# Performance work log

Measured on AMD Instinct MI355X. Metric: run time of the kernel, lower is better.

Reference implementation:

```python
import jax, jax.numpy as jnp
import numpy as np

HEAD_COUNT = 16
EMBED_DIM = 2048
B, S = 2, 2048


def setup_inputs() -> dict:
    key = jax.random.key(0)
    k1, k2, k3, k4, k5 = jax.random.split(key, 5)
    keys = jax.random.normal(k1, (B, S, EMBED_DIM), dtype=jnp.float32)
    values = jax.random.normal(k2, (B, S, EMBED_DIM), dtype=jnp.float32)
    queries = jax.random.normal(k3, (B, S, EMBED_DIM), dtype=jnp.float32)
    # padding-style mask; guarantee at least one valid key per batch row
    attention_mask = jax.random.randint(k4, (B, S), 0, 2).astype(bool)
    attention_mask = attention_mask.at[:, 0].set(True)
    w_out = jax.random.normal(k5, (EMBED_DIM, EMBED_DIM), dtype=jnp.float32) * (EMBED_DIM ** -0.5)
    return {"keys": keys, "values": values, "queries": queries,
            "attention_mask": attention_mask, "w_out": w_out}


def reference(keys, values, queries, attention_mask, w_out):
    b, s, e = queries.shape
    h = HEAD_COUNT
    c = e // h  # head dim
    k = keys.reshape(b, s, h, c)
    v = values.reshape(b, s, h, c)
    q = queries.reshape(b, s, h, c) * (c ** -0.5)
    # [B,H,Q,K] scores + additive padding bias on key axis
    scores = jnp.einsum('bqhc,bkhc->bhqk', q, k)
    bias = jnp.where(attention_mask, 0.0, -jnp.inf)[:, None, None, :]
    weights = jax.nn.softmax(scores + bias, axis=-1)
    out = jnp.einsum('bhqk,bkhc->bqhc', weights, v).reshape(b, s, e)
    # nn.Linear(bias=False): y = x @ W^T
    return out @ w_out.T
```

## Files before the change

### kernel.cpp

```cpp
#include <hip/hip_runtime.h>
#include <hip/hip_bf16.h>
#include <math.h>

#define B_ 2
#define S_ 2048
#define E_ 2048
#define H_ 16
#define C_ 128

typedef __attribute__((ext_vector_type(8))) short s8v;
typedef __attribute__((ext_vector_type(4))) float f32x4;
typedef __attribute__((ext_vector_type(2))) unsigned u32x2;
typedef __attribute__((ext_vector_type(4))) unsigned u32x4;

#define MFMA16(a, b, c) __builtin_amdgcn_mfma_f32_16x16x32_bf16((a), (b), (c), 0, 0, 0)

__device__ __forceinline__ unsigned fbits(float f) {
    union { float f; unsigned u; } v{f};
    return v.u;
}
__device__ __forceinline__ short f2bfh(float f) {
    return (short)((fbits(f) + 0x8000u) >> 16);
}
__device__ __forceinline__ unsigned bfpack(float lo, float hi) {
    return __builtin_amdgcn_perm(fbits(hi) + 0x8000u, fbits(lo) + 0x8000u, 0x07060302u);
}

__device__ __forceinline__ void glds16(const void* g, void* l) {
    __builtin_amdgcn_global_load_lds(
        (const __attribute__((address_space(1))) void*)g,
        (__attribute__((address_space(3))) void*)l, 16, 0, 0);
}

template <bool DOK>
__global__ __launch_bounds__(256) void prep_kv(
    const float* __restrict__ K, const float* __restrict__ V,
    short* __restrict__ Kb, short* __restrict__ Vt)
{
    __shared__ __align__(16) short vt[C_][66];
    const int t  = threadIdx.x;
    const int s0 = blockIdx.x * 64;
    const int bh = blockIdx.y;
    const int b = bh >> 4, h = bh & 15;

    if (DOK) {
#pragma unroll
        for (int i = 0; i < 8; ++i) {
            int idx = t + i * 256;
            int s = idx >> 5, c4 = idx & 31;
            float4 v = *(const float4*)(K + ((size_t)(b * S_ + s0 + s)) * E_ + h * C_ + c4 * 4);
            u32x2 o = {bfpack(v.x, v.y), bfpack(v.z, v.w)};
            *(u32x2*)(Kb + ((size_t)(bh * S_ + s0 + s)) * C_ + c4 * 4) = o;
        }
    }
#pragma unroll
    for (int i = 0; i < 8; ++i) {
        int idx = t + i * 256;
        int r = idx >> 5, c4 = idx & 31;
        float4 v = *(const float4*)(V + ((size_t)(b * S_ + s0 + r)) * E_ + h * C_ + c4 * 4);
        vt[c4 * 4 + 0][r] = f2bfh(v.x);
        vt[c4 * 4 + 1][r] = f2bfh(v.y);
        vt[c4 * 4 + 2][r] = f2bfh(v.z);
        vt[c4 * 4 + 3][r] = f2bfh(v.w);
    }
    __syncthreads();
#pragma unroll
    for (int i = 0; i < 4; ++i) {
        int idx = t + i * 256;
        int c = idx >> 3, sc = idx & 7;
        *(s8v*)(Vt + ((size_t)(bh * C_ + c)) * S_ + s0 + sc * 8) = *(const s8v*)&vt[c][sc * 8];
    }
}

__global__ __launch_bounds__(256) void convw_kernel(
    const float* __restrict__ W, short* __restrict__ Wb)
{
    size_t i = ((size_t)blockIdx.x * 256 + threadIdx.x) * 8;
    float4 a = *(const float4*)(W + i);
    float4 b = *(const float4*)(W + i + 4);
    u32x4 o = {bfpack(a.x, a.y), bfpack(a.z, a.w), bfpack(b.x, b.y), bfpack(b.z, b.w)};
    *(u32x4*)(Wb + i) = o;
}

constexpr int QT = 128;
constexpr int KT = 64;
constexpr float M0 = 16.0f;

template <bool KBF16>
__global__ __launch_bounds__(256, 2) void attn_mfma(
    const short* __restrict__ Kb, const float* __restrict__ Kf,
    const float* __restrict__ Qp, const short* __restrict__ Vt,
    const int* __restrict__ maskp, short* __restrict__ Op)
{
    __shared__ __align__(16) short ks[2][KT * 128];
    __shared__ __align__(16) short vs[2][C_ * 64];
    __shared__ __align__(16) short ps[4][16][72];

    const int t = threadIdx.x;
    const int w = t >> 6, lane = t & 63;
    const int c15 = lane & 15, quad = lane >> 4;
    const int q0 = blockIdx.x * QT;
    const int h = blockIdx.y, b = blockIdx.z;
    const int bh = b * H_ + h;

    const float qscale = 0.12751744458187936f;
    s8v qf[2][4];
#pragma unroll
    for (int mi = 0; mi < 2; ++mi) {
        const float* qrow = Qp + ((size_t)(b * S_ + q0 + w * 32 + mi * 16 + c15)) * E_ + h * C_;
#pragma unroll
        for (int kk = 0; kk < 4; ++kk) {
            const float* p = qrow + kk * 32 + quad * 8;
            float4 x0 = *(const float4*)p;
            float4 x1 = *(const float4*)(p + 4);
            u32x4 pk = {bfpack(x0.x * qscale, x0.y * qscale),
                        bfpack(x0.z * qscale, x0.w * qscale),
                        bfpack(x1.x * qscale, x1.y * qscale),
                        bfpack(x1.z * qscale, x1.w * qscale)};
            qf[mi][kk] = *(s8v*)&pk;
        }
    }

    s8v ones;
#pragma unroll
    for (int j = 0; j < 8; ++j) ones[j] = (short)0x3F80;

    f32x4 O[2][8], Ol[2];
#pragma unroll
    for (int mi = 0; mi < 2; ++mi) {
        Ol[mi] = (f32x4){0.f, 0.f, 0.f, 0.f};
#pragma unroll
        for (int ct = 0; ct < 8; ++ct) O[mi][ct] = (f32x4){0.f, 0.f, 0.f, 0.f};
    }

    const short* Kbh = Kb + (size_t)(bh * S_) * C_;
    const float* Kfh = Kf + (size_t)(b * S_) * E_ + h * C_;
    const short* Vbh = Vt + (size_t)(bh * C_) * S_;
    const int*   mptr = maskp + b * S_ + 4 * c15;

    int kgp[4], vgp[2];
#pragma unroll
    for (int kk = 0; kk < 4; ++kk) kgp[kk] = ((4 * kk + quad) ^ c15) * 8;
#pragma unroll
    for (int ks2 = 0; ks2 < 2; ++ks2) vgp[ks2] = ((4 * ks2 + quad) ^ (c15 & 7)) * 8;

    auto stage = [&](short* ksb, short* vsb, int k0) {
        const int r4 = lane >> 4, gp = lane & 15;
#pragma unroll
        for (int i = 0; i < 4; ++i) {
            int row = w * 16 + i * 4 + r4;
            int g = gp ^ ((row >> 2) & 15);
            glds16(Kbh + (size_t)(k0 + row) * C_ + g * 8, ksb + (w * 16 + i * 4) * 128);
        }
        const int cr = lane >> 3, gp7 = lane & 7;
#pragma unroll
        for (int i = 0; i < 4; ++i) {
            int c = w * 32 + i * 8 + cr;
            int g = gp7 ^ (c & 7);
            glds16(Vbh + (size_t)c * S_ + k0 + g * 8, vsb + (w * 32 + i * 8) * 64);
        }
    };

    auto compute = [&](const short* ksc, const short* vsc, int4 mv) {
        float bva[4] = {mv.x ? -M0 : -1e30f, mv.y ? -M0 : -1e30f,
                        mv.z ? -M0 : -1e30f, mv.w ? -M0 : -1e30f};
        f32x4 Sf[2][4];
        __builtin_amdgcn_s_setprio(1);
#pragma unroll
        for (int nt = 0; nt < 4; ++nt) {
            f32x4 s0 = (f32x4){bva[nt], bva[nt], bva[nt], bva[nt]};
            f32x4 s1 = s0;
            const short* krow = ksc + (4 * c15 + nt) * 128;
#pragma unroll
            for (int kk = 0; kk < 4; ++kk) {
                s8v bf = *(const s8v*)(krow + kgp[kk]);
                s0 = MFMA16(qf[0][kk], bf, s0);
                s1 = MFMA16(qf[1][kk], bf, s1);
            }
            Sf[0][nt] = s0; Sf[1][nt] = s1;
        }
        __builtin_amdgcn_s_setprio(0);

        s8v af[2][2];
#pragma unroll
        for (int mi = 0; mi < 2; ++mi) {
#pragma unroll
            for (int r = 0; r < 4; ++r) {
                float p0 = exp2f(Sf[mi][0][r]);
                float p1 = exp2f(Sf[mi][1][r]);
                float p2 = exp2f(Sf[mi][2][r]);
                float p3 = exp2f(Sf[mi][3][r]);
                u32x2 d = {bfpack(p0, p1), bfpack(p2, p3)};
                *(u32x2*)&ps[w][quad * 4 + r][4 * c15] = d;
            }
#pragma unroll
            for (int ks2 = 0; ks2 < 2; ++ks2)
                af[mi][ks2] = *(const s8v*)&ps[w][c15][ks2 * 32 + quad * 8];
        }

        __builtin_amdgcn_s_setprio(1);
#pragma unroll
        for (int ct = 0; ct < 8; ++ct) {
            const short* vrow = vsc + (ct * 16 + c15) * 64;
#pragma unroll
            for (int ks2 = 0; ks2 < 2; ++ks2) {
                s8v bf = *(const s8v*)(vrow + vgp[ks2]);
                O[0][ct] = MFMA16(af[0][ks2], bf, O[0][ct]);
                O[1][ct] = MFMA16(af[1][ks2], bf, O[1][ct]);
            }
        }
#pragma unroll
        for (int mi = 0; mi < 2; ++mi) {
            Ol[mi] = MFMA16(af[mi][0], ones, Ol[mi]);
            Ol[mi] = MFMA16(af[mi][1], ones, Ol[mi]);
        }
        __builtin_amdgcn_s_setprio(0);
    };

    if (KBF16) {
        stage(&ks[0][0], &vs[0][0], 0);
        int4 mcur = *(const int4*)mptr;
        __syncthreads();
#pragma unroll 1
        for (int k0 = 0; k0 < S_; k0 += 2 * KT) {
            stage(&ks[1][0], &vs[1][0], k0 + KT);
            int4 m1 = *(const int4*)(mptr + k0 + KT);
            compute(&ks[0][0], &vs[0][0], mcur);
            __syncthreads();

            int4 m2 = m1;
            if (k0 + 2 * KT < S_) {
                stage(&ks[0][0], &vs[0][0], k0 + 2 * KT);
                m2 = *(const int4*)(mptr + k0 + 2 * KT);
            }
            compute(&ks[1][0], &vs[1][0], m1);
            mcur = m2;
            __syncthreads();
        }
    } else {
#pragma unroll 1
        for (int k0 = 0; k0 < S_; k0 += KT) {
#pragma unroll
            for (int i = 0; i < 8; ++i) {
                int idx = t + i * 256;
                int r = idx >> 5, c4 = idx & 31;
                float4 kv = *(const float4*)(Kfh + (size_t)(k0 + r) * E_ + c4 * 4);
                u32x2 sv = {bfpack(kv.x, kv.y), bfpack(kv.z, kv.w)};
                int gpw = (c4 >> 1) ^ ((r >> 2) & 15);
                *(u32x2*)&ks[0][r * 128 + gpw * 8 + (c4 & 1) * 4] = sv;
            }
            {
                const int cr = lane >> 3, gp7 = lane & 7;
#pragma unroll
                for (int i = 0; i < 4; ++i) {
                    int c = w * 32 + i * 8 + cr;
                    int g = gp7 ^ (c & 7);
                    glds16(Vbh + (size_t)c * S_ + k0 + g * 8, &vs[0][(w * 32 + i * 8) * 64]);
                }
            }
            int4 mv = *(const int4*)(mptr + k0);
            __syncthreads();
            compute(&ks[0][0], &vs[0][0], mv);
            __syncthreads();
        }
    }

#pragma unroll
    for (int mi = 0; mi < 2; ++mi) {
        float inv[4];
#pragma unroll
        for (int r = 0; r < 4; ++r) inv[r] = 1.f / Ol[mi][r];
        size_t rbase = (size_t)(b * S_ + q0 + w * 32 + mi * 16 + quad * 4) * E_ + h * C_;
#pragma unroll
        for (int ct = 0; ct < 8; ++ct)
#pragma unroll
            for (int r = 0; r < 4; ++r)
                Op[rbase + (size_t)r * E_ + ct * 16 + c15] = f2bfh(O[mi][ct][r] * inv[r]);
    }
}

template <bool WBF16>
__global__ __launch_bounds__(256, 2) void proj_mfma(
    const short* __restrict__ X, const short* __restrict__ Wb,
    const float* __restrict__ Wf, float* __restrict__ Y)
{
    __shared__ __align__(16) short As[2][128 * 64];
    __shared__ __align__(16) short Bs[2][128 * 64];

    const int t = threadIdx.x;
    const int w = t >> 6, lane = t & 63;
    const int c15 = lane & 15, quad = lane >> 4;
    const int bm = blockIdx.x * 128, bn = blockIdx.y * 128;
    const int wm = (w >> 1) * 64, wn = (w & 1) * 64;

    f32x4 acc[4][4];
#pragma unroll
    for (int mi = 0; mi < 4; ++mi)
#pragma unroll
        for (int ni = 0; ni < 4; ++ni) acc[mi][ni] = (f32x4){0.f, 0.f, 0.f, 0.f};

    int agp[2];
#pragma unroll
    for (int kk = 0; kk < 2; ++kk) agp[kk] = ((4 * kk + quad) ^ (c15 & 7)) * 8;

    auto stageAB = [&](short* Ab, short* Bb, int k0) {
        const int r8 = lane >> 3, gp = lane & 7;
#pragma unroll
        for (int i = 0; i < 4; ++i) {
            int row = w * 32 + i * 8 + r8;
            int g = gp ^ (row & 7);
            glds16(X + (size_t)(bm + row) * E_ + k0 + g * 8, Ab + (w * 32 + i * 8) * 64);
            glds16(Wb + (size_t)(bn + row) * E_ + k0 + g * 8, Bb + (w * 32 + i * 8) * 64);
        }
    };

    auto compute = [&](const short* Ab, const short* Bb) {
#pragma unroll
        for (int kk = 0; kk < 2; ++kk) {
            s8v a[4], bb[4];
#pragma unroll
            for (int mi = 0; mi < 4; ++mi)
                a[mi] = *(const s8v*)(Ab + (wm + mi * 16 + c15) * 64 + agp[kk]);
#pragma unroll
            for (int ni = 0; ni < 4; ++ni)
                bb[ni] = *(const s8v*)(Bb + (wn + ni * 16 + c15) * 64 + agp[kk]);
#pragma unroll
            for (int mi = 0; mi < 4; ++mi)
#pragma unroll
                for (int ni = 0; ni < 4; ++ni)
                    acc[mi][ni] = MFMA16(a[mi], bb[ni], acc[mi][ni]);
        }
    };

    if (WBF16) {
        stageAB(&As[0][0], &Bs[0][0], 0);
        __syncthreads();
#pragma unroll 1
        for (int k0 = 0; k0 < E_; k0 += 128) {
            stageAB(&As[1][0], &Bs[1][0], k0 + 64);
            compute(&As[0][0], &Bs[0][0]);
            __syncthreads();

            if (k0 + 128 < E_) stageAB(&As[0][0], &Bs[0][0], k0 + 128);
            compute(&As[1][0], &Bs[1][0]);
            __syncthreads();
        }
    } else {
#pragma unroll 1
        for (int k0 = 0; k0 < E_; k0 += 64) {
            {
                const int r8 = lane >> 3, gp = lane & 7;
#pragma unroll
                for (int i = 0; i < 4; ++i) {
                    int row = w * 32 + i * 8 + r8;
                    int g = gp ^ (row & 7);
                    glds16(X + (size_t)(bm + row) * E_ + k0 + g * 8, &As[0][(w * 32 + i * 8) * 64]);
                }
            }
#pragma unroll
            for (int i = 0; i < 8; ++i) {
                int idx = t + i * 256;
                int r = idx >> 4, c4 = idx & 15;
                float4 wv = *(const float4*)(Wf + (size_t)(bn + r) * E_ + k0 + c4 * 4);
                u32x2 sv = {bfpack(wv.x, wv.y), bfpack(wv.z, wv.w)};
                int gpw = (c4 >> 1) ^ (r & 7);
                *(u32x2*)&Bs[0][r * 64 + gpw * 8 + (c4 & 1) * 4] = sv;
            }
            __syncthreads();
            compute(&As[0][0], &Bs[0][0]);
            __syncthreads();
        }
    }

#pragma unroll
    for (int mi = 0; mi < 4; ++mi)
#pragma unroll
        for (int ni = 0; ni < 4; ++ni) {
            size_t rbase = (size_t)(bm + wm + mi * 16 + quad * 4) * E_ + bn + wn + ni * 16 + c15;
#pragma unroll
            for (int r = 0; r < 4; ++r) Y[rbase + (size_t)r * E_] = acc[mi][ni][r];
        }
}

extern "C" void kernel_launch(void* const* d_in, const int* in_sizes, int n_in,
                              void* d_out, int out_size, void* d_ws, size_t ws_size,
                              hipStream_t stream) {
    const float* keys    = (const float*)d_in[0];
    const float* values  = (const float*)d_in[1];
    const float* queries = (const float*)d_in[2];
    const int*   mask    = (const int*)d_in[3];
    const float* w_out   = (const float*)d_in[4];
    float* out = (float*)d_out;

    const size_t EL = (size_t)B_ * S_ * E_;
    short* ws  = (short*)d_ws;
    short* VtW = ws;
    short* Xb  = ws + EL;
    short* Kb  = ws + 2 * EL;
    short* Wb  = ws + 3 * EL;

    const bool hasK = ws_size >= (3 * EL) * 2;
    const bool hasW = ws_size >= (3 * EL + (size_t)E_ * E_) * 2;

    if (hasK)
        prep_kv<true><<<dim3(S_ / 64, B_ * H_), 256, 0, stream>>>(keys, values, Kb, VtW);
    else
        prep_kv<false><<<dim3(S_ / 64, B_ * H_), 256, 0, stream>>>(keys, values, Kb, VtW);
    if (hasW) convw_kernel<<<(E_ * E_ / 8) / 256, 256, 0, stream>>>(w_out, Wb);

    if (hasK)
        attn_mfma<true><<<dim3(S_ / QT, H_, B_), 256, 0, stream>>>(Kb, keys, queries, VtW, mask, Xb);
    else
        attn_mfma<false><<<dim3(S_ / QT, H_, B_), 256, 0, stream>>>(Kb, keys, queries, VtW, mask, Xb);

    if (hasW)
        proj_mfma<true><<<dim3((B_ * S_) / 128, E_ / 128), 256, 0, stream>>>(Xb, Wb, w_out, out);
    else
        proj_mfma<false><<<dim3((B_ * S_) / 128, E_ / 128), 256, 0, stream>>>(Xb, Wb, w_out, out);
}
```

Baseline: 281.6 us.

## Use 512-thread blocks with 16-row warps and drop K/V double buffering

The attention kernel moves from 4 waves handling 32 query rows each to 8 waves handling 16 rows each. It also replaces the double-buffered K/V LDS staging with a single buffer and two syncs per tile. The projection GEMM likewise uses 8 waves, each computing a 64x32 sub-tile. The aim is to cut registers per wave and raise occupancy, at the cost of less K-fragment reuse per wave, more syncs, and no overlap between loads and compute.

```diff
diff --git a/kernel.cpp b/kernel.cpp
--- a/kernel.cpp
+++ b/kernel.cpp
@@ -87,14 +87,14 @@
 constexpr float M0 = 16.0f;
 
 template <bool KBF16>
-__global__ __launch_bounds__(256, 2) void attn_mfma(
+__global__ __launch_bounds__(512, 4) void attn_mfma(
     const short* __restrict__ Kb, const float* __restrict__ Kf,
     const float* __restrict__ Qp, const short* __restrict__ Vt,
     const int* __restrict__ maskp, short* __restrict__ Op)
 {
-    __shared__ __align__(16) short ks[2][KT * 128];
-    __shared__ __align__(16) short vs[2][C_ * 64];
-    __shared__ __align__(16) short ps[4][16][72];
+    __shared__ __align__(16) short ks[KT * 128];
+    __shared__ __align__(16) short vs[C_ * 64];
+    __shared__ __align__(16) short ps[8][16][72];
 
     const int t = threadIdx.x;
     const int w = t >> 6, lane = t & 63;
@@ -104,10 +104,9 @@
     const int bh = b * H_ + h;
 
     const float qscale = 0.12751744458187936f;
-    s8v qf[2][4];
-#pragma unroll
-    for (int mi = 0; mi < 2; ++mi) {
-        const float* qrow = Qp + ((size_t)(b * S_ + q0 + w * 32 + mi * 16 + c15)) * E_ + h * C_;
+    s8v qf[4];
+    {
+        const float* qrow = Qp + ((size_t)(b * S_ + q0 + w * 16 + c15)) * E_ + h * C_;
 #pragma unroll
         for (int kk = 0; kk < 4; ++kk) {
             const float* p = qrow + kk * 32 + quad * 8;
@@ -117,7 +116,7 @@
                         bfpack(x0.z * qscale, x0.w * qscale),
                         bfpack(x1.x * qscale, x1.y * qscale),
                         bfpack(x1.z * qscale, x1.w * qscale)};
-            qf[mi][kk] = *(s8v*)&pk;
+            qf[kk] = *(s8v*)&pk;
         }
     }
 
@@ -125,13 +124,10 @@
 #pragma unroll
     for (int j = 0; j < 8; ++j) ones[j] = (short)0x3F80;
 
-    f32x4 O[2][8], Ol[2];
-#pragma unroll
-    for (int mi = 0; mi < 2; ++mi) {
-        Ol[mi] = (f32x4){0.f, 0.f, 0.f, 0.f};
-#pragma unroll
-        for (int ct = 0; ct < 8; ++ct) O[mi][ct] = (f32x4){0.f, 0.f, 0.f, 0.f};
-    }
+    f32x4 O[8], Ol;
+    Ol = (f32x4){0.f, 0.f, 0.f, 0.f};
+#pragma unroll
+    for (int ct = 0; ct < 8; ++ct) O[ct] = (f32x4){0.f, 0.f, 0.f, 0.f};
 
     const short* Kbh = Kb + (size_t)(bh * S_) * C_;
     const float* Kfh = Kf + (size_t)(b * S_) * E_ + h * C_;
@@ -144,143 +140,101 @@
 #pragma unroll
     for (int ks2 = 0; ks2 < 2; ++ks2) vgp[ks2] = ((4 * ks2 + quad) ^ (c15 & 7)) * 8;
 
-    auto stage = [&](short* ksb, short* vsb, int k0) {
-        const int r4 = lane >> 4, gp = lane & 15;
-#pragma unroll
-        for (int i = 0; i < 4; ++i) {
-            int row = w * 16 + i * 4 + r4;
-            int g = gp ^ ((row >> 2) & 15);
-            glds16(Kbh + (size_t)(k0 + row) * C_ + g * 8, ksb + (w * 16 + i * 4) * 128);
-        }
-        const int cr = lane >> 3, gp7 = lane & 7;
-#pragma unroll
-        for (int i = 0; i < 4; ++i) {
-            int c = w * 32 + i * 8 + cr;
-            int g = gp7 ^ (c & 7);
-            glds16(Vbh + (size_t)c * S_ + k0 + g * 8, vsb + (w * 32 + i * 8) * 64);
-        }
-    };
-
-    auto compute = [&](const short* ksc, const short* vsc, int4 mv) {
-        float bva[4] = {mv.x ? -M0 : -1e30f, mv.y ? -M0 : -1e30f,
-                        mv.z ? -M0 : -1e30f, mv.w ? -M0 : -1e30f};
-        f32x4 Sf[2][4];
-        __builtin_amdgcn_s_setprio(1);
-#pragma unroll
-        for (int nt = 0; nt < 4; ++nt) {
-            f32x4 s0 = (f32x4){bva[nt], bva[nt], bva[nt], bva[nt]};
-            f32x4 s1 = s0;
-            const short* krow = ksc + (4 * c15 + nt) * 128;
-#pragma unroll
-            for (int kk = 0; kk < 4; ++kk) {
-                s8v bf = *(const s8v*)(krow + kgp[kk]);
-                s0 = MFMA16(qf[0][kk], bf, s0);
-                s1 = MFMA16(qf[1][kk], bf, s1);
-            }
-            Sf[0][nt] = s0; Sf[1][nt] = s1;
-        }
-        __builtin_amdgcn_s_setprio(0);
-
-        s8v af[2][2];
-#pragma unroll
-        for (int mi = 0; mi < 2; ++mi) {
-#pragma unroll
-            for (int r = 0; r < 4; ++r) {
-                float p0 = exp2f(Sf[mi][0][r]);
-                float p1 = exp2f(Sf[mi][1][r]);
-                float p2 = exp2f(Sf[mi][2][r]);
-                float p3 = exp2f(Sf[mi][3][r]);
-                u32x2 d = {bfpack(p0, p1), bfpack(p2, p3)};
-                *(u32x2*)&ps[w][quad * 4 + r][4 * c15] = d;
-            }
-#pragma unroll
-            for (int ks2 = 0; ks2 < 2; ++ks2)
-                af[mi][ks2] = *(const s8v*)&ps[w][c15][ks2 * 32 + quad * 8];
-        }
-
-        __builtin_amdgcn_s_setprio(1);
-#pragma unroll
-        for (int ct = 0; ct < 8; ++ct) {
-            const short* vrow = vsc + (ct * 16 + c15) * 64;
-#pragma unroll
-            for (int ks2 = 0; ks2 < 2; ++ks2) {
-                s8v bf = *(const s8v*)(vrow + vgp[ks2]);
-                O[0][ct] = MFMA16(af[0][ks2], bf, O[0][ct]);
-                O[1][ct] = MFMA16(af[1][ks2], bf, O[1][ct]);
-            }
-        }
-#pragma unroll
-        for (int mi = 0; mi < 2; ++mi) {
-            Ol[mi] = MFMA16(af[mi][0], ones, Ol[mi]);
-            Ol[mi] = MFMA16(af[mi][1], ones, Ol[mi]);
-        }
-        __builtin_amdgcn_s_setprio(0);
-    };
-
-    if (KBF16) {
-        stage(&ks[0][0], &vs[0][0], 0);
-        int4 mcur = *(const int4*)mptr;
-        __syncthreads();
 #pragma unroll 1
-        for (int k0 = 0; k0 < S_; k0 += 2 * KT) {
-            stage(&ks[1][0], &vs[1][0], k0 + KT);
-            int4 m1 = *(const int4*)(mptr + k0 + KT);
-            compute(&ks[0][0], &vs[0][0], mcur);
-            __syncthreads();
-
-            int4 m2 = m1;
-            if (k0 + 2 * KT < S_) {
-                stage(&ks[0][0], &vs[0][0], k0 + 2 * KT);
-                m2 = *(const int4*)(mptr + k0 + 2 * KT);
-            }
-            compute(&ks[1][0], &vs[1][0], m1);
-            mcur = m2;
-            __syncthreads();
-        }
-    } else {
-#pragma unroll 1
-        for (int k0 = 0; k0 < S_; k0 += KT) {
-#pragma unroll
-            for (int i = 0; i < 8; ++i) {
-                int idx = t + i * 256;
+    for (int k0 = 0; k0 < S_; k0 += KT) {
+        if (KBF16) {
+            const int r4 = lane >> 4, gp = lane & 15;
+#pragma unroll
+            for (int i = 0; i < 2; ++i) {
+                int row = w * 8 + i * 4 + r4;
+                int g = gp ^ ((row >> 2) & 15);
+                glds16(Kbh + (size_t)(k0 + row) * C_ + g * 8, &ks[(w * 8 + i * 4) * 128]);
+            }
+        } else {
+#pragma unroll
+            for (int i = 0; i < 4; ++i) {
+                int idx = t + i * 512;
                 int r = idx >> 5, c4 = idx & 31;
                 float4 kv = *(const float4*)(Kfh + (size_t)(k0 + r) * E_ + c4 * 4);
                 u32x2 sv = {bfpack(kv.x, kv.y), bfpack(kv.z, kv.w)};
                 int gpw = (c4 >> 1) ^ ((r >> 2) & 15);
-                *(u32x2*)&ks[0][r * 128 + gpw * 8 + (c4 & 1) * 4] = sv;
-            }
-            {
-                const int cr = lane >> 3, gp7 = lane & 7;
-#pragma unroll
-                for (int i = 0; i < 4; ++i) {
-                    int c = w * 32 + i * 8 + cr;
-                    int g = gp7 ^ (c & 7);
-                    glds16(Vbh + (size_t)c * S_ + k0 + g * 8, &vs[0][(w * 32 + i * 8) * 64]);
-                }
-            }
-            int4 mv = *(const int4*)(mptr + k0);
-            __syncthreads();
-            compute(&ks[0][0], &vs[0][0], mv);
-            __syncthreads();
-        }
-    }
-
-#pragma unroll
-    for (int mi = 0; mi < 2; ++mi) {
+                *(u32x2*)&ks[r * 128 + gpw * 8 + (c4 & 1) * 4] = sv;
+            }
+        }
+        {
+            const int cr = lane >> 3, gp7 = lane & 7;
+#pragma unroll
+            for (int i = 0; i < 2; ++i) {
+                int c = w * 16 + i * 8 + cr;
+                int g = gp7 ^ (c & 7);
+                glds16(Vbh + (size_t)c * S_ + k0 + g * 8, &vs[(w * 16 + i * 8) * 64]);
+            }
+        }
+        int4 mv = *(const int4*)(mptr + k0);
+        __syncthreads();
+
+        float bva[4] = {mv.x ? -M0 : -1e30f, mv.y ? -M0 : -1e30f,
+                        mv.z ? -M0 : -1e30f, mv.w ? -M0 : -1e30f};
+        f32x4 Sf[4];
+        __builtin_amdgcn_s_setprio(1);
+#pragma unroll
+        for (int nt = 0; nt < 4; ++nt) {
+            f32x4 s0 = (f32x4){bva[nt], bva[nt], bva[nt], bva[nt]};
+            const short* krow = &ks[(4 * c15 + nt) * 128];
+#pragma unroll
+            for (int kk = 0; kk < 4; ++kk) {
+                s8v bf = *(const s8v*)(krow + kgp[kk]);
+                s0 = MFMA16(qf[kk], bf, s0);
+            }
+            Sf[nt] = s0;
+        }
+        __builtin_amdgcn_s_setprio(0);
+
+#pragma unroll
+        for (int r = 0; r < 4; ++r) {
+            float p0 = exp2f(Sf[0][r]);
+            float p1 = exp2f(Sf[1][r]);
+            float p2 = exp2f(Sf[2][r]);
+            float p3 = exp2f(Sf[3][r]);
+            u32x2 d = {bfpack(p0, p1), bfpack(p2, p3)};
+            *(u32x2*)&ps[w][quad * 4 + r][4 * c15] = d;
+        }
+        s8v af[2];
+#pragma unroll
+        for (int ks2 = 0; ks2 < 2; ++ks2)
+            af[ks2] = *(const s8v*)&ps[w][c15][ks2 * 32 + quad * 8];
+
+        __builtin_amdgcn_s_setprio(1);
+#pragma unroll
+        for (int ct = 0; ct < 8; ++ct) {
+            const short* vrow = &vs[(ct * 16 + c15) * 64];
+#pragma unroll
+            for (int ks2 = 0; ks2 < 2; ++ks2) {
+                s8v bf = *(const s8v*)(vrow + vgp[ks2]);
+                O[ct] = MFMA16(af[ks2], bf, O[ct]);
+            }
+        }
+        Ol = MFMA16(af[0], ones, Ol);
+        Ol = MFMA16(af[1], ones, Ol);
+        __builtin_amdgcn_s_setprio(0);
+        __syncthreads();
+    }
+
+    {
         float inv[4];
 #pragma unroll
-        for (int r = 0; r < 4; ++r) inv[r] = 1.f / Ol[mi][r];
-        size_t rbase = (size_t)(b * S_ + q0 + w * 32 + mi * 16 + quad * 4) * E_ + h * C_;
+        for (int r = 0; r < 4; ++r) inv[r] = 1.f / Ol[r];
+        size_t rbase = (size_t)(b * S_ + q0 + w * 16 + quad * 4) * E_ + h * C_;
 #pragma unroll
         for (int ct = 0; ct < 8; ++ct)
 #pragma unroll
             for (int r = 0; r < 4; ++r)
-                Op[rbase + (size_t)r * E_ + ct * 16 + c15] = f2bfh(O[mi][ct][r] * inv[r]);
+                Op[rbase + (size_t)r * E_ + ct * 16 + c15] = f2bfh(O[ct][r] * inv[r]);
     }
 }
 
 template <bool WBF16>
-__global__ __launch_bounds__(256, 2) void proj_mfma(
+__global__ __launch_bounds__(512, 4) void proj_mfma(
     const short* __restrict__ X, const short* __restrict__ Wb,
     const float* __restrict__ Wf, float* __restrict__ Y)
 {
@@ -291,13 +245,13 @@
     const int w = t >> 6, lane = t & 63;
     const int c15 = lane & 15, quad = lane >> 4;
     const int bm = blockIdx.x * 128, bn = blockIdx.y * 128;
-    const int wm = (w >> 1) * 64, wn = (w & 1) * 64;
-
-    f32x4 acc[4][4];
+    const int wm = (w >> 2) * 64, wn = (w & 3) * 32;
+
+    f32x4 acc[4][2];
 #pragma unroll
     for (int mi = 0; mi < 4; ++mi)
 #pragma unroll
-        for (int ni = 0; ni < 4; ++ni) acc[mi][ni] = (f32x4){0.f, 0.f, 0.f, 0.f};
+        for (int ni = 0; ni < 2; ++ni) acc[mi][ni] = (f32x4){0.f, 0.f, 0.f, 0.f};
 
     int agp[2];
 #pragma unroll
@@ -306,28 +260,28 @@
     auto stageAB = [&](short* Ab, short* Bb, int k0) {
         const int r8 = lane >> 3, gp = lane & 7;
 #pragma unroll
-        for (int i = 0; i < 4; ++i) {
-            int row = w * 32 + i * 8 + r8;
+        for (int i = 0; i < 2; ++i) {
+            int row = w * 16 + i * 8 + r8;
             int g = gp ^ (row & 7);
-            glds16(X + (size_t)(bm + row) * E_ + k0 + g * 8, Ab + (w * 32 + i * 8) * 64);
-            glds16(Wb + (size_t)(bn + row) * E_ + k0 + g * 8, Bb + (w * 32 + i * 8) * 64);
+            glds16(X + (size_t)(bm + row) * E_ + k0 + g * 8, Ab + (w * 16 + i * 8) * 64);
+            glds16(Wb + (size_t)(bn + row) * E_ + k0 + g * 8, Bb + (w * 16 + i * 8) * 64);
         }
     };
 
     auto compute = [&](const short* Ab, const short* Bb) {
 #pragma unroll
         for (int kk = 0; kk < 2; ++kk) {
-            s8v a[4], bb[4];
+            s8v a[4], bb[2];
 #pragma unroll
             for (int mi = 0; mi < 4; ++mi)
                 a[mi] = *(const s8v*)(Ab + (wm + mi * 16 + c15) * 64 + agp[kk]);
 #pragma unroll
-            for (int ni = 0; ni < 4; ++ni)
+            for (int ni = 0; ni < 2; ++ni)
                 bb[ni] = *(const s8v*)(Bb + (wn + ni * 16 + c15) * 64 + agp[kk]);
 #pragma unroll
             for (int mi = 0; mi < 4; ++mi)
 #pragma unroll
-                for (int ni = 0; ni < 4; ++ni)
+                for (int ni = 0; ni < 2; ++ni)
                     acc[mi][ni] = MFMA16(a[mi], bb[ni], acc[mi][ni]);
         }
     };
@@ -351,15 +305,15 @@
             {
                 const int r8 = lane >> 3, gp = lane & 7;
 #pragma unroll
-                for (int i = 0; i < 4; ++i) {
-                    int row = w * 32 + i * 8 + r8;
+                for (int i = 0; i < 2; ++i) {
+                    int row = w * 16 + i * 8 + r8;
                     int g = gp ^ (row & 7);
-                    glds16(X + (size_t)(bm + row) * E_ + k0 + g * 8, &As[0][(w * 32 + i * 8) * 64]);
+                    glds16(X + (size_t)(bm + row) * E_ + k0 + g * 8, &As[0][(w * 16 + i * 8) * 64]);
                 }
             }
 #pragma unroll
-            for (int i = 0; i < 8; ++i) {
-                int idx = t + i * 256;
+            for (int i = 0; i < 4; ++i) {
+                int idx = t + i * 512;
                 int r = idx >> 4, c4 = idx & 15;
                 float4 wv = *(const float4*)(Wf + (size_t)(bn + r) * E_ + k0 + c4 * 4);
                 u32x2 sv = {bfpack(wv.x, wv.y), bfpack(wv.z, wv.w)};
@@ -375,7 +329,7 @@
 #pragma unroll
     for (int mi = 0; mi < 4; ++mi)
 #pragma unroll
-        for (int ni = 0; ni < 4; ++ni) {
+        for (int ni = 0; ni < 2; ++ni) {
             size_t rbase = (size_t)(bm + wm + mi * 16 + quad * 4) * E_ + bn + wn + ni * 16 + c15;
 #pragma unroll
             for (int r = 0; r < 4; ++r) Y[rbase + (size_t)r * E_] = acc[mi][ni][r];
@@ -409,12 +363,12 @@
     if (hasW) convw_kernel<<<(E_ * E_ / 8) / 256, 256, 0, stream>>>(w_out, Wb);
 
     if (hasK)
-        attn_mfma<true><<<dim3(S_ / QT, H_, B_), 256, 0, stream>>>(Kb, keys, queries, VtW, mask, Xb);
+        attn_mfma<true><<<dim3(S_ / QT, H_, B_), 512, 0, stream>>>(Kb, keys, queries, VtW, mask, Xb);
     else
-        attn_mfma<false><<<dim3(S_ / QT, H_, B_), 256, 0, stream>>>(Kb, keys, queries, VtW, mask, Xb);
+        attn_mfma<false><<<dim3(S_ / QT, H_, B_), 512, 0, stream>>>(Kb, keys, queries, VtW, mask, Xb);
 
     if (hasW)
-        proj_mfma<true><<<dim3((B_ * S_) / 128, E_ / 128), 256, 0, stream>>>(Xb, Wb, w_out, out);
+        proj_mfma<true><<<dim3((B_ * S_) / 128, E_ / 128), 512, 0, stream>>>(Xb, Wb, w_out, out);
     else
-        proj_mfma<false><<<dim3((B_ * S_) / 128, E_ / 128), 256, 0, stream>>>(Xb, Wb, w_out, out);
-}
+        proj_mfma<false><<<dim3((B_ * S_) / 128, E_ / 128), 512, 0, stream>>>(Xb, Wb, w_out, out);
+}
```

Result: no change. 276.7 us (-1.7%).
